# Kernel tuning notes

Measured on AMD Instinct MI355X. Metric: run time of the kernel, lower is better.

## Reference

```python
import jax, jax.numpy as jnp
import numpy as np

B, D, S = 4096, 1024, 1024

def setup_inputs() -> dict:
    key = jax.random.key(0)
    ks = jax.random.split(key, 12)
    u = lambda k, shp: jax.random.uniform(k, shp, jnp.float32, -0.05, 0.05)
    return {
        "inputs": jax.random.normal(ks[0], (B, D), jnp.float32),
        "h0": jax.random.normal(ks[1], (B, S), jnp.float32),
        "c0": jax.random.normal(ks[2], (B, S), jnp.float32),
        "w_f": u(ks[3], (D, S)), "u_f": u(ks[4], (S, S)), "b_f": u(ks[5], (S,)),
        "w_i": u(ks[6], (D, S)), "u_i": u(ks[7], (S, S)), "b_i": u(ks[8], (S,)),
        "w_o": u(ks[9], (D, S)), "u_o": u(ks[10], (S, S)), "b_o": u(ks[11], (S,)),
    }

def reference(inputs, h0, c0, w_f, u_f, b_f, w_i, u_i, b_i, w_o, u_o, b_o):
    # Faithful to the original: input_cell reuses the FORGET gate weights and
    # sigmoid (not tanh, not w_c) -- a quirk of the source module.
    pre_f = inputs @ w_f + h0 @ u_f + b_f          # [B, S]
    forget_gate = jax.nn.sigmoid(pre_f)
    input_gate = jax.nn.sigmoid(inputs @ w_i + h0 @ u_i + b_i)
    output_gate = jax.nn.sigmoid(inputs @ w_o + h0 @ u_o + b_o)
    input_cell = jax.nn.sigmoid(pre_f)             # same pre-activation as forget gate
    c_new = forget_gate * c0 + input_cell * input_gate
    h_new = output_gate * jnp.tanh(c_new)
    return (h_new, c_new)
```

## Files before the change

### kernel.cpp

```cpp
#include <hip/hip_runtime.h>
#include <cstdint>
#include <cstddef>


typedef __attribute__((ext_vector_type(8))) short bf16x8;
typedef __attribute__((ext_vector_type(4))) float f32x4;
typedef __attribute__((ext_vector_type(8))) short s16x8;
typedef __attribute__((ext_vector_type(4))) float f32x4v;

#define MROWS 4096
#define KDIM  1024
#define NCOLS 1024

__device__ __forceinline__ short f2bf(float f) {
    uint32_t u = __builtin_bit_cast(uint32_t, f);
    u += 0x7fffu + ((u >> 16) & 1u);
    return (short)(u >> 16);
}

__global__ void cvt_bf16_kernel(const float* __restrict__ x,
                                const float* __restrict__ h,
                                short* __restrict__ xb,
                                short* __restrict__ hb) {
    int b = blockIdx.x;
    const float* in;
    short* out;
    if (b < 2048) { in = x; out = xb; }
    else          { in = h; out = hb; b -= 2048; }
    const int i = (b * 256 + threadIdx.x) * 8;
    f32x4v a = *(const f32x4v*)(in + i);
    f32x4v c = *(const f32x4v*)(in + i + 4);
    s16x8 o;
    o[0] = f2bf(a[0]); o[1] = f2bf(a[1]); o[2] = f2bf(a[2]); o[3] = f2bf(a[3]);
    o[4] = f2bf(c[0]); o[5] = f2bf(c[1]); o[6] = f2bf(c[2]); o[7] = f2bf(c[3]);
    *(s16x8*)(out + i) = o;
}

struct W6 {
    const float* src[6];
    short* dst[6];
};

__global__ void transpose_cvt_kernel(W6 p) {
    __shared__ short tile[32][33];
    const float* __restrict__ w  = p.src[blockIdx.z];
    short* __restrict__       wt = p.dst[blockIdx.z];
    const int tx = threadIdx.x & 31;
    const int ty = threadIdx.x >> 5;
    const int kbase = blockIdx.y * 32;
    const int nbase = blockIdx.x * 32;
#pragma unroll
    for (int r = 0; r < 4; ++r) {
        int k = kbase + ty + r * 8;
        tile[ty + r * 8][tx] = f2bf(w[k * NCOLS + nbase + tx]);
    }
    __syncthreads();
#pragma unroll
    for (int r = 0; r < 4; ++r) {
        int n = nbase + ty + r * 8;
        wt[n * KDIM + kbase + tx] = tile[tx][ty + r * 8];
    }
}

__global__ __launch_bounds__(512)
void lstm_gemm_kernel(const short* __restrict__ Xb, const short* __restrict__ Hb,
                      const short* __restrict__ WT0, const short* __restrict__ WT1,
                      const short* __restrict__ WT2,
                      const short* __restrict__ UT0, const short* __restrict__ UT1,
                      const short* __restrict__ UT2,
                      const float* __restrict__ bf_, const float* __restrict__ bi_,
                      const float* __restrict__ bo_,
                      const float* __restrict__ c0,
                      float* __restrict__ outH, float* __restrict__ outC) {
    __shared__ __align__(16) short lds[2][16384];

    const int tid  = threadIdx.x;
    const int lane = tid & 63;
    const int wave = tid >> 6;
    const int wm   = wave >> 2;
    const int wn   = wave & 3;
    const int m0   = blockIdx.y * 128;
    const int n0   = blockIdx.x * 128;

    const int l15 = lane & 15;
    const int q   = lane >> 4;

    f32x4 acc[3][4][2] = {};

    const int srow   = tid >> 2;
    const int schunk = (tid & 3) ^ ((tid >> 3) & 3);
    const int skoff  = schunk * 8;

    int aOff[4], bOff[2];
#pragma unroll
    for (int m = 0; m < 4; ++m) {
        const int row = wm * 64 + m * 16 + l15;
        aOff[m] = row * 64 + ((q ^ ((row >> 1) & 3)) << 4);
    }
#pragma unroll
    for (int n = 0; n < 2; ++n) {
        const int row = wn * 32 + n * 16 + l15;
        bOff[n] = row * 64 + ((q ^ ((row >> 1) & 3)) << 4);
    }

    auto stage = [&](int buf, int kt) {
        const bool second = kt >= 32;
        const short* aS = second ? Hb  : Xb;
        const short* s0 = second ? UT0 : WT0;
        const short* s1 = second ? UT1 : WT1;
        const short* s2 = second ? UT2 : WT2;
        const int kk = (kt & 31) * 32 + skoff;
#pragma unroll
        for (int r = 0; r < 4; ++r) {
            const short* src = (r == 0) ? aS : (r == 1 ? s0 : (r == 2 ? s1 : s2));
            const int rbase = (r == 0) ? m0 : n0;
            const char* g = (const char*)(src + (size_t)(rbase + srow) * KDIM + kk);
            __builtin_amdgcn_global_load_lds(
                (const __attribute__((address_space(1))) unsigned int*)(uintptr_t)g,
                (__attribute__((address_space(3))) unsigned int*)(uintptr_t)
                    ((char*)&lds[buf][0] + r * 8192 + tid * 16),
                16, 0, 0);
        }
    };

    stage(0, 0);
    __syncthreads();

    int buf = 0;
    for (int kt = 0; kt < 64; ++kt) {
        if (kt < 63) stage(buf ^ 1, kt + 1);

        const char* L = (const char*)&lds[buf][0];
        bf16x8 af[4];
#pragma unroll
        for (int m = 0; m < 4; ++m)
            af[m] = *(const bf16x8*)(L + aOff[m]);
#pragma unroll
        for (int g3 = 0; g3 < 3; ++g3) {
#pragma unroll
            for (int n = 0; n < 2; ++n) {
                bf16x8 bv = *(const bf16x8*)(L + 8192 * (1 + g3) + bOff[n]);
#pragma unroll
                for (int m = 0; m < 4; ++m)
                    acc[g3][m][n] = __builtin_amdgcn_mfma_f32_16x16x32_bf16(
                        af[m], bv, acc[g3][m][n], 0, 0, 0);
            }
        }
        __syncthreads();
        buf ^= 1;
    }

    const int rj = (lane >> 4) * 4;
#pragma unroll
    for (int m = 0; m < 4; ++m) {
#pragma unroll
        for (int n = 0; n < 2; ++n) {
            const int col = n0 + wn * 32 + n * 16 + l15;
            const float bfv = bf_[col], biv = bi_[col], bov = bo_[col];
            const f32x4 pf = acc[0][m][n];
            const f32x4 pi = acc[1][m][n];
            const f32x4 po = acc[2][m][n];
#pragma unroll
            for (int j = 0; j < 4; ++j) {
                const int row = m0 + wm * 64 + m * 16 + rj + j;
                const float fg = 1.f / (1.f + __expf(-(pf[j] + bfv)));
                const float ig = 1.f / (1.f + __expf(-(pi[j] + biv)));
                const float og = 1.f / (1.f + __expf(-(po[j] + bov)));
                const float cv = c0[row * NCOLS + col];
                const float cn = fg * cv + fg * ig;
                const float e  = __expf(-2.f * cn);
                const float th = (1.f - e) / (1.f + e);
                outH[row * NCOLS + col] = og * th;
                outC[row * NCOLS + col] = cn;
            }
        }
    }
}

extern "C" void kernel_launch(void* const* d_in, const int* in_sizes, int n_in,
                              void* d_out, int out_size, void* d_ws, size_t ws_size,
                              hipStream_t stream) {
    const float* inputs = (const float*)d_in[0];
    const float* h0     = (const float*)d_in[1];
    const float* c0     = (const float*)d_in[2];
    const float* w_f    = (const float*)d_in[3];
    const float* u_f    = (const float*)d_in[4];
    const float* b_f    = (const float*)d_in[5];
    const float* w_i    = (const float*)d_in[6];
    const float* u_i    = (const float*)d_in[7];
    const float* b_i    = (const float*)d_in[8];
    const float* w_o    = (const float*)d_in[9];
    const float* u_o    = (const float*)d_in[10];
    const float* b_o    = (const float*)d_in[11];

    float* outH = (float*)d_out;
    float* outC = outH + (size_t)MROWS * NCOLS;

    char* ws = (char*)d_ws;
    short* Xb  = (short*)(ws);
    short* Hb  = (short*)(ws + (8u << 20));
    short* WT0 = (short*)(ws + (16u << 20));
    short* WT1 = (short*)(ws + (18u << 20));
    short* WT2 = (short*)(ws + (20u << 20));
    short* UT0 = (short*)(ws + (22u << 20));
    short* UT1 = (short*)(ws + (24u << 20));
    short* UT2 = (short*)(ws + (26u << 20));

    cvt_bf16_kernel<<<4096, 256, 0, stream>>>(inputs, h0, Xb, Hb);

    W6 p;
    p.src[0] = w_f; p.src[1] = w_i; p.src[2] = w_o;
    p.src[3] = u_f; p.src[4] = u_i; p.src[5] = u_o;
    p.dst[0] = WT0; p.dst[1] = WT1; p.dst[2] = WT2;
    p.dst[3] = UT0; p.dst[4] = UT1; p.dst[5] = UT2;
    transpose_cvt_kernel<<<dim3(32, 32, 6), 256, 0, stream>>>(p);

    dim3 grid(NCOLS / 128, MROWS / 128);
    lstm_gemm_kernel<<<grid, 512, 0, stream>>>(
        Xb, Hb, WT0, WT1, WT2, UT0, UT1, UT2,
        b_f, b_i, b_o, c0, outH, outC);
}
```

Before: 84.71 us.

## Shrink GEMM block to 128x64 tile with 256 threads for two blocks per CU

The fused LSTM GEMM block tile drops from 128x128 (512 threads) to 128x64 (256 threads, 4 waves). The LDS stage buffers shrink to match, and launch bounds ask for two blocks per CU so more blocks can be resident and overlap barrier stalls. s_setprio is also raised around the MFMA section. The grid doubles to 512 blocks, and the smaller N tile lowers A-tile reuse, so each block streams the X/H rows again for half as many output columns.

Result: faster. 79.33 us (-6.4%).

```diff
diff --git a/kernel.cpp b/kernel.cpp
--- a/kernel.cpp
+++ b/kernel.cpp
@@ -62,7 +62,7 @@
     }
 }
 
-__global__ __launch_bounds__(512)
+__global__ __launch_bounds__(256, 2)
 void lstm_gemm_kernel(const short* __restrict__ Xb, const short* __restrict__ Hb,
                       const short* __restrict__ WT0, const short* __restrict__ WT1,
                       const short* __restrict__ WT2,
@@ -72,24 +72,23 @@
                       const float* __restrict__ bo_,
                       const float* __restrict__ c0,
                       float* __restrict__ outH, float* __restrict__ outC) {
-    __shared__ __align__(16) short lds[2][16384];
+    __shared__ __align__(16) short lds[2][10240];
 
     const int tid  = threadIdx.x;
     const int lane = tid & 63;
     const int wave = tid >> 6;
-    const int wm   = wave >> 2;
-    const int wn   = wave & 3;
+    const int wm   = wave >> 1;
+    const int wn   = wave & 1;
     const int m0   = blockIdx.y * 128;
-    const int n0   = blockIdx.x * 128;
+    const int n0   = blockIdx.x * 64;
 
     const int l15 = lane & 15;
     const int q   = lane >> 4;
 
     f32x4 acc[3][4][2] = {};
 
-    const int srow   = tid >> 2;
-    const int schunk = (tid & 3) ^ ((tid >> 3) & 3);
-    const int skoff  = schunk * 8;
+    const int srow  = tid >> 2;
+    const int skoff = ((tid & 3) ^ ((tid >> 3) & 3)) * 8;
 
     int aOff[4], bOff[2];
 #pragma unroll
@@ -106,19 +105,29 @@
     auto stage = [&](int buf, int kt) {
         const bool second = kt >= 32;
         const short* aS = second ? Hb  : Xb;
-        const short* s0 = second ? UT0 : WT0;
-        const short* s1 = second ? UT1 : WT1;
-        const short* s2 = second ? UT2 : WT2;
+        const short* b0 = second ? UT0 : WT0;
+        const short* b1 = second ? UT1 : WT1;
+        const short* b2 = second ? UT2 : WT2;
         const int kk = (kt & 31) * 32 + skoff;
-#pragma unroll
-        for (int r = 0; r < 4; ++r) {
-            const short* src = (r == 0) ? aS : (r == 1 ? s0 : (r == 2 ? s1 : s2));
-            const int rbase = (r == 0) ? m0 : n0;
-            const char* g = (const char*)(src + (size_t)(rbase + srow) * KDIM + kk);
+        char* Lb = (char*)&lds[buf][0];
+        const char* gA0 = (const char*)(aS + (size_t)(m0 + srow) * KDIM + kk);
+        const char* gA1 = (const char*)(aS + (size_t)(m0 + srow + 64) * KDIM + kk);
+        __builtin_amdgcn_global_load_lds(
+            (const __attribute__((address_space(1))) unsigned int*)(uintptr_t)gA0,
+            (__attribute__((address_space(3))) unsigned int*)(uintptr_t)(Lb + tid * 16),
+            16, 0, 0);
+        __builtin_amdgcn_global_load_lds(
+            (const __attribute__((address_space(1))) unsigned int*)(uintptr_t)gA1,
+            (__attribute__((address_space(3))) unsigned int*)(uintptr_t)(Lb + 4096 + tid * 16),
+            16, 0, 0);
+#pragma unroll
+        for (int g = 0; g < 3; ++g) {
+            const short* bS = (g == 0) ? b0 : (g == 1 ? b1 : b2);
+            const char* gB = (const char*)(bS + (size_t)(n0 + srow) * KDIM + kk);
             __builtin_amdgcn_global_load_lds(
-                (const __attribute__((address_space(1))) unsigned int*)(uintptr_t)g,
+                (const __attribute__((address_space(1))) unsigned int*)(uintptr_t)gB,
                 (__attribute__((address_space(3))) unsigned int*)(uintptr_t)
-                    ((char*)&lds[buf][0] + r * 8192 + tid * 16),
+                    (Lb + 8192 + g * 4096 + tid * 16),
                 16, 0, 0);
         }
     };
@@ -126,28 +135,28 @@
     stage(0, 0);
     __syncthreads();
 
-    int buf = 0;
     for (int kt = 0; kt < 64; ++kt) {
-        if (kt < 63) stage(buf ^ 1, kt + 1);
-
-        const char* L = (const char*)&lds[buf][0];
+        if (kt < 63) stage((kt + 1) & 1, kt + 1);
+
+        const char* L = (const char*)&lds[kt & 1][0];
         bf16x8 af[4];
 #pragma unroll
         for (int m = 0; m < 4; ++m)
             af[m] = *(const bf16x8*)(L + aOff[m]);
-#pragma unroll
-        for (int g3 = 0; g3 < 3; ++g3) {
+        __builtin_amdgcn_s_setprio(1);
+#pragma unroll
+        for (int g = 0; g < 3; ++g) {
 #pragma unroll
             for (int n = 0; n < 2; ++n) {
-                bf16x8 bv = *(const bf16x8*)(L + 8192 * (1 + g3) + bOff[n]);
+                bf16x8 bv = *(const bf16x8*)(L + 8192 + g * 4096 + bOff[n]);
 #pragma unroll
                 for (int m = 0; m < 4; ++m)
-                    acc[g3][m][n] = __builtin_amdgcn_mfma_f32_16x16x32_bf16(
-                        af[m], bv, acc[g3][m][n], 0, 0, 0);
+                    acc[g][m][n] = __builtin_amdgcn_mfma_f32_16x16x32_bf16(
+                        af[m], bv, acc[g][m][n], 0, 0, 0);
             }
         }
+        __builtin_amdgcn_s_setprio(0);
         __syncthreads();
-        buf ^= 1;
     }
 
     const int rj = (lane >> 4) * 4;
@@ -215,8 +224,8 @@
     p.dst[3] = UT0; p.dst[4] = UT1; p.dst[5] = UT2;
     transpose_cvt_kernel<<<dim3(32, 32, 6), 256, 0, stream>>>(p);
 
-    dim3 grid(NCOLS / 128, MROWS / 128);
-    lstm_gemm_kernel<<<grid, 512, 0, stream>>>(
+    dim3 grid(NCOLS / 64, MROWS / 128);
+    lstm_gemm_kernel<<<grid, 256, 0, stream>>>(
         Xb, Hb, WT0, WT1, WT2, UT0, UT1, UT2,
         b_f, b_i, b_o, c0, outH, outC);
 }
```

## Pack concatenated X|H and gate-interleaved weights; 256x192 tiles with phased pipeline

Applied to the files above, without the earlier changes.

Activations are written as one concatenated [B, 2048] bf16 matrix. The three gates' weights are packed into a single K=2048 matrix with the gate columns interleaved in groups of 16, so one B tile covers all three gates for 64 output columns. The GEMM tile grows to 256 rows by 192 packed columns with a K step of 64, and the main loop is split into four phases that issue global-to-LDS loads between MFMA groups, using explicit barriers, waitcnts and setprio. The aim is more data reuse per LDS byte and better overlap of loads with MFMA work, at the cost of 112KB of LDS, a smaller grid of 256 blocks, and fragile hand-written synchronization.

Result: faster. 76.22 us (-10.0%).

```diff
diff --git a/kernel.cpp b/kernel.cpp
--- a/kernel.cpp
+++ b/kernel.cpp
@@ -9,8 +9,9 @@
 typedef __attribute__((ext_vector_type(4))) float f32x4v;
 
 #define MROWS 4096
-#define KDIM  1024
-#define NCOLS 1024
+#define KD    1024
+#define KALL  2048
+#define NC    1024
 
 __device__ __forceinline__ short f2bf(float f) {
     uint32_t u = __builtin_bit_cast(uint32_t, f);
@@ -20,31 +21,30 @@
 
 __global__ void cvt_bf16_kernel(const float* __restrict__ x,
                                 const float* __restrict__ h,
-                                short* __restrict__ xb,
-                                short* __restrict__ hb) {
+                                short* __restrict__ ab) {
     int b = blockIdx.x;
     const float* in;
-    short* out;
-    if (b < 2048) { in = x; out = xb; }
-    else          { in = h; out = hb; b -= 2048; }
+    int coff;
+    if (b < 2048) { in = x; coff = 0; }
+    else          { in = h; coff = KD; b -= 2048; }
     const int i = (b * 256 + threadIdx.x) * 8;
+    const int row = i >> 10, col = i & 1023;
     f32x4v a = *(const f32x4v*)(in + i);
     f32x4v c = *(const f32x4v*)(in + i + 4);
     s16x8 o;
     o[0] = f2bf(a[0]); o[1] = f2bf(a[1]); o[2] = f2bf(a[2]); o[3] = f2bf(a[3]);
     o[4] = f2bf(c[0]); o[5] = f2bf(c[1]); o[6] = f2bf(c[2]); o[7] = f2bf(c[3]);
-    *(s16x8*)(out + i) = o;
-}
-
-struct W6 {
-    const float* src[6];
-    short* dst[6];
-};
-
-__global__ void transpose_cvt_kernel(W6 p) {
+    *(s16x8*)(ab + (size_t)row * KALL + coff + col) = o;
+}
+
+struct W6 { const float* src[6]; };
+
+__global__ void pack_w_kernel(W6 p, short* __restrict__ bp) {
     __shared__ short tile[32][33];
-    const float* __restrict__ w  = p.src[blockIdx.z];
-    short* __restrict__       wt = p.dst[blockIdx.z];
+    const int z = blockIdx.z;
+    const float* __restrict__ w = p.src[z];
+    const int g    = (z < 3) ? z : z - 3;
+    const int koff = (z < 3) ? 0 : KD;
     const int tx = threadIdx.x & 31;
     const int ty = threadIdx.x >> 5;
     const int kbase = blockIdx.y * 32;
@@ -52,129 +52,223 @@
 #pragma unroll
     for (int r = 0; r < 4; ++r) {
         int k = kbase + ty + r * 8;
-        tile[ty + r * 8][tx] = f2bf(w[k * NCOLS + nbase + tx]);
+        tile[ty + r * 8][tx] = f2bf(w[k * NC + nbase + tx]);
     }
     __syncthreads();
 #pragma unroll
     for (int r = 0; r < 4; ++r) {
-        int n = nbase + ty + r * 8;
-        wt[n * KDIM + kbase + tx] = tile[tx][ty + r * 8];
-    }
-}
-
-__global__ __launch_bounds__(512)
-void lstm_gemm_kernel(const short* __restrict__ Xb, const short* __restrict__ Hb,
-                      const short* __restrict__ WT0, const short* __restrict__ WT1,
-                      const short* __restrict__ WT2,
-                      const short* __restrict__ UT0, const short* __restrict__ UT1,
-                      const short* __restrict__ UT2,
+        const int n = nbase + ty + r * 8;
+        const int pcol = ((n >> 4) * 3 + g) * 16 + (n & 15);
+        bp[(size_t)pcol * KALL + koff + kbase + tx] = tile[tx][ty + r * 8];
+    }
+}
+
+__global__ __launch_bounds__(512, 2)
+void lstm_gemm_kernel(const short* __restrict__ Ab, const short* __restrict__ Bp,
                       const float* __restrict__ bf_, const float* __restrict__ bi_,
                       const float* __restrict__ bo_,
                       const float* __restrict__ c0,
                       float* __restrict__ outH, float* __restrict__ outC) {
-    __shared__ __align__(16) short lds[2][16384];
+    __shared__ __align__(16) char lds[2][57344];
 
     const int tid  = threadIdx.x;
     const int lane = tid & 63;
     const int wave = tid >> 6;
-    const int wm   = wave >> 2;
-    const int wn   = wave & 3;
-    const int m0   = blockIdx.y * 128;
-    const int n0   = blockIdx.x * 128;
+    const int wr   = wave >> 2;
+    const int wc   = wave & 3;
+    const int m0   = blockIdx.y * 256;
+    const int np0  = blockIdx.x * 192;
 
     const int l15 = lane & 15;
     const int q   = lane >> 4;
 
-    f32x4 acc[3][4][2] = {};
-
-    const int srow   = tid >> 2;
-    const int schunk = (tid & 3) ^ ((tid >> 3) & 3);
-    const int skoff  = schunk * 8;
-
-    int aOff[4], bOff[2];
-#pragma unroll
-    for (int m = 0; m < 4; ++m) {
-        const int row = wm * 64 + m * 16 + l15;
-        aOff[m] = row * 64 + ((q ^ ((row >> 1) & 3)) << 4);
-    }
-#pragma unroll
-    for (int n = 0; n < 2; ++n) {
-        const int row = wn * 32 + n * 16 + l15;
-        bOff[n] = row * 64 + ((q ^ ((row >> 1) & 3)) << 4);
-    }
-
-    auto stage = [&](int buf, int kt) {
-        const bool second = kt >= 32;
-        const short* aS = second ? Hb  : Xb;
-        const short* s0 = second ? UT0 : WT0;
-        const short* s1 = second ? UT1 : WT1;
-        const short* s2 = second ? UT2 : WT2;
-        const int kk = (kt & 31) * 32 + skoff;
-#pragma unroll
-        for (int r = 0; r < 4; ++r) {
-            const short* src = (r == 0) ? aS : (r == 1 ? s0 : (r == 2 ? s1 : s2));
-            const int rbase = (r == 0) ? m0 : n0;
-            const char* g = (const char*)(src + (size_t)(rbase + srow) * KDIM + kk);
-            __builtin_amdgcn_global_load_lds(
-                (const __attribute__((address_space(1))) unsigned int*)(uintptr_t)g,
-                (__attribute__((address_space(3))) unsigned int*)(uintptr_t)
-                    ((char*)&lds[buf][0] + r * 8192 + tid * 16),
-                16, 0, 0);
+    f32x4 acc[8][3] = {};
+
+    const int srow = tid >> 2;
+    const int skel = ((tid & 3) ^ ((tid >> 3) & 3)) * 8;
+    const short* aPtr[4];
+#pragma unroll
+    for (int l = 0; l < 4; ++l) {
+        const int ks = l >> 1, mh = l & 1;
+        aPtr[l] = Ab + (size_t)(m0 + mh * 128 + srow) * KALL + ks * 32 + skel;
+    }
+    const short* bPtr[3];
+#pragma unroll
+    for (int w = 0; w < 3; ++w) {
+        const int pbyte = w * 8192 + tid * 16;
+        const int ks  = pbyte / 12288;
+        const int rem = pbyte - ks * 12288;
+        const int row = rem >> 6;
+        const int slot = (rem >> 4) & 3;
+        bPtr[w] = Bp + (size_t)(np0 + row) * KALL + ks * 32 +
+                  ((slot ^ ((row >> 1) & 3)) * 8);
+    }
+
+    int aOffV[8];
+#pragma unroll
+    for (int m = 0; m < 8; ++m) {
+        const int r = m * 16 + l15;
+        aOffV[m] = wr * 8192 + r * 64 + ((q ^ ((r >> 1) & 3)) << 4);
+    }
+    int bOffV[3];
+#pragma unroll
+    for (int g = 0; g < 3; ++g) {
+        const int r = wc * 48 + g * 16 + l15;
+        bOffV[g] = 32768 + r * 64 + ((q ^ ((r >> 1) & 3)) << 4);
+    }
+
+#define GLDS(SRC, DOFF)                                                      \
+    __builtin_amdgcn_global_load_lds(                                        \
+        (const __attribute__((address_space(1))) unsigned int*)(uintptr_t)(SRC), \
+        (__attribute__((address_space(3))) unsigned int*)(uintptr_t)         \
+            (Ls + (DOFF) + tid * 16), 16, 0, 0)
+
+#define BAR    __builtin_amdgcn_s_barrier()
+#define SCHED0 __builtin_amdgcn_sched_barrier(0)
+#define LGKM0  asm volatile("s_waitcnt lgkmcnt(0)" ::: "memory")
+
+#define MFMA12(MB)                                                           \
+    {                                                                        \
+        __builtin_amdgcn_s_setprio(1);                                       \
+        _Pragma("unroll")                                                    \
+        for (int mm = 0; mm < 4; ++mm)                                       \
+            _Pragma("unroll")                                                \
+            for (int g = 0; g < 3; ++g)                                      \
+                acc[(MB) + mm][g] = __builtin_amdgcn_mfma_f32_16x16x32_bf16( \
+                    af[mm], bg[g], acc[(MB) + mm][g], 0, 0, 0);              \
+        __builtin_amdgcn_s_setprio(0);                                       \
+    }
+
+    {
+        char* Ls = lds[0];
+        GLDS(aPtr[0], 0);      GLDS(aPtr[1], 8192);
+        GLDS(bPtr[0], 32768);  GLDS(bPtr[1], 40960);
+        GLDS(aPtr[2], 16384);  GLDS(aPtr[3], 24576);
+        GLDS(bPtr[2], 49152);
+    }
+    asm volatile("s_waitcnt vmcnt(3)" ::: "memory");
+    BAR;
+
+    bf16x8 af[4], bg[3];
+
+    for (int t = 0; t < 31; ++t) {
+        const char* L = lds[t & 1];
+        char* Ls = lds[(t + 1) & 1];
+        const int kb = (t + 1) * 64;
+
+#pragma unroll
+        for (int mm = 0; mm < 4; ++mm) af[mm] = *(const bf16x8*)(L + aOffV[mm]);
+#pragma unroll
+        for (int g = 0; g < 3; ++g)    bg[g] = *(const bf16x8*)(L + bOffV[g]);
+        GLDS(aPtr[0] + kb, 0);
+        GLDS(aPtr[1] + kb, 8192);
+        SCHED0;
+        BAR;
+        LGKM0;
+        SCHED0;
+        MFMA12(0);
+        BAR;
+
+#pragma unroll
+        for (int mm = 0; mm < 4; ++mm)
+            af[mm] = *(const bf16x8*)(L + aOffV[4 + mm]);
+        GLDS(bPtr[0] + kb, 32768);
+        GLDS(bPtr[1] + kb, 40960);
+        SCHED0;
+        BAR;
+        LGKM0;
+        SCHED0;
+        MFMA12(4);
+        asm volatile("s_waitcnt vmcnt(4)" ::: "memory");
+        BAR;
+
+#pragma unroll
+        for (int mm = 0; mm < 4; ++mm)
+            af[mm] = *(const bf16x8*)(L + 16384 + aOffV[mm]);
+#pragma unroll
+        for (int g = 0; g < 3; ++g)
+            bg[g] = *(const bf16x8*)(L + 12288 + bOffV[g]);
+        GLDS(aPtr[2] + kb, 16384);
+        GLDS(aPtr[3] + kb, 24576);
+        SCHED0;
+        BAR;
+        LGKM0;
+        SCHED0;
+        MFMA12(0);
+        BAR;
+
+#pragma unroll
+        for (int mm = 0; mm < 4; ++mm)
+            af[mm] = *(const bf16x8*)(L + 16384 + aOffV[4 + mm]);
+        GLDS(bPtr[2] + kb, 49152);
+        SCHED0;
+        BAR;
+        LGKM0;
+        SCHED0;
+        MFMA12(4);
+        asm volatile("s_waitcnt vmcnt(3)" ::: "memory");
+        BAR;
+    }
+
+    {
+        const char* L = lds[1];
+#pragma unroll
+        for (int mm = 0; mm < 4; ++mm) af[mm] = *(const bf16x8*)(L + aOffV[mm]);
+#pragma unroll
+        for (int g = 0; g < 3; ++g)    bg[g] = *(const bf16x8*)(L + bOffV[g]);
+        SCHED0; BAR; LGKM0; SCHED0;
+        MFMA12(0);
+        BAR;
+#pragma unroll
+        for (int mm = 0; mm < 4; ++mm)
+            af[mm] = *(const bf16x8*)(L + aOffV[4 + mm]);
+        SCHED0; BAR; LGKM0; SCHED0;
+        MFMA12(4);
+        asm volatile("s_waitcnt vmcnt(0)" ::: "memory");
+        BAR;
+#pragma unroll
+        for (int mm = 0; mm < 4; ++mm)
+            af[mm] = *(const bf16x8*)(L + 16384 + aOffV[mm]);
+#pragma unroll
+        for (int g = 0; g < 3; ++g)
+            bg[g] = *(const bf16x8*)(L + 12288 + bOffV[g]);
+        SCHED0; BAR; LGKM0; SCHED0;
+        MFMA12(0);
+        BAR;
+#pragma unroll
+        for (int mm = 0; mm < 4; ++mm)
+            af[mm] = *(const bf16x8*)(L + 16384 + aOffV[4 + mm]);
+        LGKM0; SCHED0;
+        MFMA12(4);
+    }
+
+    const int rj  = q * 4;
+    const int col = blockIdx.x * 64 + wc * 16 + l15;
+    const float bfv = bf_[col], biv = bi_[col], bov = bo_[col];
+#pragma unroll
+    for (int m = 0; m < 8; ++m) {
+        const f32x4 pf = acc[m][0];
+        const f32x4 pi = acc[m][1];
+        const f32x4 po = acc[m][2];
+#pragma unroll
+        for (int j = 0; j < 4; ++j) {
+            const int row = m0 + wr * 128 + m * 16 + rj + j;
+            const float fg = 1.f / (1.f + __expf(-(pf[j] + bfv)));
+            const float ig = 1.f / (1.f + __expf(-(pi[j] + biv)));
+            const float og = 1.f / (1.f + __expf(-(po[j] + bov)));
+            const float cv = c0[row * NC + col];
+            const float cn = fg * cv + fg * ig;
+            const float e  = __expf(-2.f * cn);
+            const float th = (1.f - e) / (1.f + e);
+            outH[row * NC + col] = og * th;
+            outC[row * NC + col] = cn;
         }
-    };
-
-    stage(0, 0);
-    __syncthreads();
-
-    int buf = 0;
-    for (int kt = 0; kt < 64; ++kt) {
-        if (kt < 63) stage(buf ^ 1, kt + 1);
-
-        const char* L = (const char*)&lds[buf][0];
-        bf16x8 af[4];
-#pragma unroll
-        for (int m = 0; m < 4; ++m)
-            af[m] = *(const bf16x8*)(L + aOff[m]);
-#pragma unroll
-        for (int g3 = 0; g3 < 3; ++g3) {
-#pragma unroll
-            for (int n = 0; n < 2; ++n) {
-                bf16x8 bv = *(const bf16x8*)(L + 8192 * (1 + g3) + bOff[n]);
-#pragma unroll
-                for (int m = 0; m < 4; ++m)
-                    acc[g3][m][n] = __builtin_amdgcn_mfma_f32_16x16x32_bf16(
-                        af[m], bv, acc[g3][m][n], 0, 0, 0);
-            }
-        }
-        __syncthreads();
-        buf ^= 1;
-    }
-
-    const int rj = (lane >> 4) * 4;
-#pragma unroll
-    for (int m = 0; m < 4; ++m) {
-#pragma unroll
-        for (int n = 0; n < 2; ++n) {
-            const int col = n0 + wn * 32 + n * 16 + l15;
-            const float bfv = bf_[col], biv = bi_[col], bov = bo_[col];
-            const f32x4 pf = acc[0][m][n];
-            const f32x4 pi = acc[1][m][n];
-            const f32x4 po = acc[2][m][n];
-#pragma unroll
-            for (int j = 0; j < 4; ++j) {
-                const int row = m0 + wm * 64 + m * 16 + rj + j;
-                const float fg = 1.f / (1.f + __expf(-(pf[j] + bfv)));
-                const float ig = 1.f / (1.f + __expf(-(pi[j] + biv)));
-                const float og = 1.f / (1.f + __expf(-(po[j] + bov)));
-                const float cv = c0[row * NCOLS + col];
-                const float cn = fg * cv + fg * ig;
-                const float e  = __expf(-2.f * cn);
-                const float th = (1.f - e) / (1.f + e);
-                outH[row * NCOLS + col] = og * th;
-                outC[row * NCOLS + col] = cn;
-            }
-        }
-    }
+    }
+#undef GLDS
+#undef BAR
+#undef SCHED0
+#undef LGKM0
+#undef MFMA12
 }
 
 extern "C" void kernel_launch(void* const* d_in, const int* in_sizes, int n_in,
@@ -194,29 +288,20 @@
     const float* b_o    = (const float*)d_in[11];
 
     float* outH = (float*)d_out;
-    float* outC = outH + (size_t)MROWS * NCOLS;
+    float* outC = outH + (size_t)MROWS * NC;
 
     char* ws = (char*)d_ws;
-    short* Xb  = (short*)(ws);
-    short* Hb  = (short*)(ws + (8u << 20));
-    short* WT0 = (short*)(ws + (16u << 20));
-    short* WT1 = (short*)(ws + (18u << 20));
-    short* WT2 = (short*)(ws + (20u << 20));
-    short* UT0 = (short*)(ws + (22u << 20));
-    short* UT1 = (short*)(ws + (24u << 20));
-    short* UT2 = (short*)(ws + (26u << 20));
-
-    cvt_bf16_kernel<<<4096, 256, 0, stream>>>(inputs, h0, Xb, Hb);
+    short* Ab = (short*)(ws);
+    short* Bp = (short*)(ws + (16u << 20));
+
+    cvt_bf16_kernel<<<4096, 256, 0, stream>>>(inputs, h0, Ab);
 
     W6 p;
     p.src[0] = w_f; p.src[1] = w_i; p.src[2] = w_o;
     p.src[3] = u_f; p.src[4] = u_i; p.src[5] = u_o;
-    p.dst[0] = WT0; p.dst[1] = WT1; p.dst[2] = WT2;
-    p.dst[3] = UT0; p.dst[4] = UT1; p.dst[5] = UT2;
-    transpose_cvt_kernel<<<dim3(32, 32, 6), 256, 0, stream>>>(p);
-
-    dim3 grid(NCOLS / 128, MROWS / 128);
+    pack_w_kernel<<<dim3(32, 32, 6), 256, 0, stream>>>(p, Bp);
+
+    dim3 grid(16, 16);
     lstm_gemm_kernel<<<grid, 512, 0, stream>>>(
-        Xb, Hb, WT0, WT1, WT2, UT0, UT1, UT2,
-        b_f, b_i, b_o, c0, outH, outC);
-}
+        Ab, Bp, b_f, b_i, b_o, c0, outH, outC);
+}
```
